# Kernel tuning notes

Hardware: AMD Instinct MI355X
Metric: run time of the kernel (lower is better)

## Reference

```python
import jax, jax.numpy as jnp
import numpy as np

K = 3          # kernel size
SH, SW = 2, 1  # stride
PH, PW = 1, 1  # padding


def conv2d(x, w, b, stride, pad):
    y = jax.lax.conv_general_dilated(
        x, w, window_strides=stride,
        padding=[(pad[0], pad[0]), (pad[1], pad[1])],
        dimension_numbers=('NCHW', 'OIHW', 'NCHW'))
    return y + b[None, :, None, None]


def setup_inputs() -> dict:
    key = jax.random.key(0)
    ks = jax.random.split(key, 4)
    x = jax.random.normal(ks[0], (8, 64, 128, 128), jnp.float32)
    # scale offset weights small so sampled offsets are O(1) pixels (exercises
    # the bilinear path without sampling far out of bounds)
    w_offset = jax.random.normal(ks[1], (18, 64, 3, 3), jnp.float32) * 0.02
    b_offset = jnp.zeros((18,), jnp.float32)
    w_mask = jax.random.normal(ks[2], (9, 64, 3, 3), jnp.float32) * 0.05
    b_mask = jnp.zeros((9,), jnp.float32)
    w_conv = jax.random.normal(ks[3], (64, 64, 3, 3), jnp.float32) * (1.0 / 24.0)
    return dict(x=x, w_offset=w_offset, b_offset=b_offset,
                w_mask=w_mask, b_mask=b_mask, w_conv=w_conv)


def _bilinear_gather(x, py, px):
    # x: [B,C,H,W]; py, px: [B,K2,Ho,Wo] float sampling coordinates.
    # Zero-padding outside the image (torchvision deform_conv2d semantics).
    B, C, H, W = x.shape
    y0f = jnp.floor(py)
    x0f = jnp.floor(px)
    dy = py - y0f
    dx = px - x0f
    y0 = y0f.astype(jnp.int32)
    x0 = x0f.astype(jnp.int32)

    def corner(yi, xi, wgt):
        valid = (yi >= 0) & (yi < H) & (xi >= 0) & (xi < W)
        yc = jnp.clip(yi, 0, H - 1)
        xc = jnp.clip(xi, 0, W - 1)
        # per-batch fancy gather -> [B, C, K2, Ho, Wo]
        g = jax.vmap(lambda xb, yb, xbi: xb[:, yb, xbi])(x, yc, xc)
        return g * (wgt * valid)[:, None]

    return (corner(y0,     x0,     (1 - dy) * (1 - dx))
            + corner(y0,     x0 + 1, (1 - dy) * dx)
            + corner(y0 + 1, x0,     dy * (1 - dx))
            + corner(y0 + 1, x0 + 1, dy * dx))


def reference(x, w_offset, b_offset, w_mask, b_mask, w_conv):
    B, C, H, W = x.shape
    offset = conv2d(x, w_offset, b_offset, (SH, SW), (PH, PW))   # [B, 2*K2, Ho, Wo]
    mask = jax.nn.sigmoid(conv2d(x, w_mask, b_mask, (SH, SW), (PH, PW)))  # [B, K2, Ho, Wo]
    Ho, Wo = offset.shape[2], offset.shape[3]
    K2 = K * K
    off = offset.reshape(B, K2, 2, Ho, Wo)
    off_y = off[:, :, 0]   # [B,K2,Ho,Wo]
    off_x = off[:, :, 1]
    ky = (jnp.arange(K2) // K).astype(jnp.float32)
    kx = (jnp.arange(K2) % K).astype(jnp.float32)
    hs = (jnp.arange(Ho) * SH - PH).astype(jnp.float32)
    ws = (jnp.arange(Wo) * SW - PW).astype(jnp.float32)
    py = off_y + ky[None, :, None, None] + hs[None, None, :, None]
    px = off_x + kx[None, :, None, None] + ws[None, None, None, :]
    sampled = _bilinear_gather(x, py, px) * mask[:, None]  # [B,C,K2,Ho,Wo]
    # weighted accumulate over in-channels and kernel taps
    out = jnp.einsum('ock,bckhw->bohw', w_conv.reshape(-1, C, K2), sampled)
    return out
```

## Files before the change

### kernel.cpp

```cpp
#include <hip/hip_runtime.h>
#include <hip/hip_fp16.h>
#include <math.h>

#define BB 8
#define CC 64
#define HH 128
#define WW 128
#define HO 64
#define WO 128
#define OC 64
#define HW (HH * WW)

typedef __attribute__((ext_vector_type(4))) float floatx4;
typedef __attribute__((ext_vector_type(8))) _Float16 half8;

__device__ __forceinline__ unsigned short f2h(float f) {
    __half h = __float2half(f);
    return __builtin_bit_cast(unsigned short, h);
}
__device__ __forceinline__ unsigned int packpair(float a, float b) {
    __half2 h = __floats2half2_rn(a, b);
    return __builtin_bit_cast(unsigned int, h);
}
__device__ __forceinline__ void lgkm_barrier() {
    asm volatile("s_waitcnt lgkmcnt(0)" ::: "memory");
    __builtin_amdgcn_s_barrier();
}

__global__ __launch_bounds__(256) void prep(
    const float* __restrict__ x,
    const float* __restrict__ w_off, const float* __restrict__ w_msk,
    const float* __restrict__ w_conv,
    unsigned int* __restrict__ xP,
    unsigned short* __restrict__ Wom, unsigned short* __restrict__ W2)
{
    __shared__ float T[64][77];
    int tid = threadIdx.x, bx = blockIdx.x;
    if (bx < 2048) {
        int wh = bx & 1, b = (bx >> 1) & 7, y = bx >> 4;
        int w0 = wh << 6;
        const float* xb = x + (((size_t)b * CC) * HH + y) * WW + w0;
#pragma unroll
        for (int i = 0; i < 4; ++i) {
            int idx = i * 256 + tid;
            int cch = idx >> 4, f4 = (idx & 15) << 2;
            floatx4 v = *(const floatx4*)(xb + (size_t)cch * HW + f4);
            T[cch][f4 + 0] = v.x;
            T[cch][f4 + 1] = v.y;
            T[cch][f4 + 2] = v.z;
            T[cch][f4 + 3] = v.w;
        }
        if (tid < 64) {
            float e = 0.0f;
            if (w0 + 64 < WW) e = xb[(size_t)tid * HW + 64];
            T[tid][64] = e;
        }
        __syncthreads();
        int ch = tid & 63;
        int wb = (tid >> 6) << 4;
        size_t base = ((((size_t)b * HH + y) * WW) + w0 + wb) * 64 + ch;
#pragma unroll
        for (int j = 0; j < 4; ++j) {
            int wl = wb + 4 * j;
            float a0 = T[ch][wl + 0];
            float a1 = T[ch][wl + 1];
            float a2 = T[ch][wl + 2];
            float a3 = T[ch][wl + 3];
            float a4 = T[ch][wl + 4];
            xP[base + (size_t)(4 * j + 0) * 64] = packpair(a0, a1);
            xP[base + (size_t)(4 * j + 1) * 64] = packpair(a1, a2);
            xP[base + (size_t)(4 * j + 2) * 64] = packpair(a2, a3);
            xP[base + (size_t)(4 * j + 3) * 64] = packpair(a3, a4);
        }
    } else if (bx < 2120) {
        int i = (bx - 2048) * 256 + tid;
        int chn = i / 576, kk = i % 576;
        int xs = kk >> 6, cc = kk & 63;
        float v = 0.0f;
        if (chn < 18)      v = w_off[(chn * CC + cc) * 9 + xs];
        else if (chn < 27) v = w_msk[((chn - 18) * CC + cc) * 9 + xs];
        Wom[i] = f2h(v);
    } else {
        int i = (bx - 2120) * 256 + tid;
        int k = i % 9, cc = (i / 9) % CC, o = i / (CC * 9);
        W2[((size_t)k * OC + o) * CC + cc] = f2h(w_conv[i]);
    }
}

__global__ __launch_bounds__(256, 4) void fused(
    const unsigned int* __restrict__ xP,
    const unsigned short* __restrict__ Wom, const unsigned short* __restrict__ W2,
    const float* __restrict__ b_off, const float* __restrict__ b_msk,
    float* __restrict__ out)
{
    __shared__ __align__(16) char lds[18304];
    typedef _Float16 XsRow[34][72];
    XsRow* Xs = (XsRow*)lds;
    unsigned short (*S)[32][64] = (unsigned short(*)[32][64])lds;
    uint2* metaC = (uint2*)(lds + 8192);
    uint2* metaR = (uint2*)(lds + 10496);
    float (*omr)[33] = (float(*)[33])(lds + 14720);

    int tid = threadIdx.x;
    int lane = tid & 63;
    int wv = __builtin_amdgcn_readfirstlane(tid >> 6);
    int bx = blockIdx.x;
    int b = bx & 7;
    int rest = bx >> 3;
    int h = rest >> 2;
    int w0 = (rest & 3) * 32;
    int h2 = 2 * h - 1;
    int m16 = lane & 15, q = lane >> 4;

    const unsigned int* xPb_u = xP + (size_t)b * HW * 64;

    for (int u = tid; u < 1632; u += 256) {
        int ky = u / 544;
        int rem = u - ky * 544;
        int col = rem >> 4, c4 = rem & 15;
        int hy = h2 + ky, wc = w0 - 1 + col;
        unsigned int lo0 = 0u, lo1 = 0u;
        if ((unsigned)hy < (unsigned)HH && (unsigned)wc < (unsigned)WW) {
            const uint4 g = *(const uint4*)(xPb_u + ((size_t)hy * WW + wc) * 64 + c4 * 4);
            lo0 = (g.x & 0xffffu) | (g.y << 16);
            lo1 = (g.z & 0xffffu) | (g.w << 16);
        }
        uint2* dst = (uint2*)((unsigned short*)lds + ((ky * 34 + col) * 72 + c4 * 4));
        *dst = make_uint2(lo0, lo1);
    }
    lgkm_barrier();

    {
        int mt = wv & 1, nt = wv >> 1;
        floatx4 a = (floatx4){0.f, 0.f, 0.f, 0.f};
        const _Float16* wa = (const _Float16*)Wom + (mt * 16 + m16) * 576 + q * 8;
#pragma unroll
        for (int t = 0; t < 18; ++t) {
            int xs = t >> 1, ky = xs / 3, kx = xs % 3;
            half8 af = *(const half8*)(wa + t * 32);
            half8 bf = *(const half8*)&Xs[ky][nt * 16 + m16 + kx][(t & 1) * 32 + q * 8];
            a = __builtin_amdgcn_mfma_f32_16x16x32_f16(af, bf, a, 0, 0, 0);
        }
#pragma unroll
        for (int r = 0; r < 4; ++r) {
            int chn = mt * 16 + q * 4 + r;
            if (chn < 27) omr[chn][nt * 16 + m16] = a[r];
        }
    }
    lgkm_barrier();

    for (int u = tid; u < 288; u += 256) {
        int kk = u >> 5, pos = u & 31;
        float offy = omr[2 * kk][pos] + b_off[2 * kk];
        float offx = omr[2 * kk + 1][pos] + b_off[2 * kk + 1];
        float mk = 1.0f / (1.0f + __expf(-(omr[18 + kk][pos] + b_msk[kk])));
        float py = offy + (float)(kk / 3) + (float)h2;
        float px = offx + (float)(kk % 3) + (float)(w0 + pos - 1);

        float y0f = floorf(py), x0f = floorf(px);
        float dy = py - y0f, dx = px - x0f;
        int y0 = (int)y0f, x0 = (int)x0f;
        int y1 = y0 + 1, x1 = x0 + 1;
        bool vy0 = (unsigned)y0 < (unsigned)HH;
        bool vy1 = (unsigned)y1 < (unsigned)HH;
        bool vx0 = (unsigned)x0 < (unsigned)WW;
        bool vx1 = (unsigned)x1 < (unsigned)WW;
        float w00 = (1.0f - dy) * (1.0f - dx) * ((vy0 && vx0) ? mk : 0.0f);
        float w01 = (1.0f - dy) * dx          * ((vy0 && vx1) ? mk : 0.0f);
        float w10 = dy * (1.0f - dx)          * ((vy1 && vx0) ? mk : 0.0f);
        float w11 = dy * dx                   * ((vy1 && vx1) ? mk : 0.0f);
        int xbase = min(max(x0, 0), WW - 2);
        bool s0 = x0 > xbase;
        bool s1 = x1 > xbase;
        float cxA = (s0 ? 0.f : w00) + (s1 ? 0.f : w01);
        float cyA = (s0 ? w00 : 0.f) + (s1 ? w01 : 0.f);
        float cxB = (s0 ? 0.f : w10) + (s1 ? 0.f : w11);
        float cyB = (s0 ? w10 : 0.f) + (s1 ? w11 : 0.f);
        int yc0 = min(max(y0, 0), HH - 1);
        int yc1 = min(max(y1, 0), HH - 1);

        __half2 hA = __floats2half2_rn(cxA, cyA);
        __half2 hB = __floats2half2_rn(cxB, cyB);
        metaC[u] = make_uint2(__builtin_bit_cast(unsigned int, hA),
                              __builtin_bit_cast(unsigned int, hB));
        metaR[u] = make_uint2((unsigned)(yc0 * WW + xbase) * 256u,
                              (unsigned)(yc1 * WW + xbase) * 256u);
    }
    lgkm_barrier();

    int p0 = wv * 8;
    const char* xPb = (const char*)xPb_u;
    unsigned int voff = 4u * (unsigned)lane;
    floatx4 acc0 = (floatx4){0.f, 0.f, 0.f, 0.f};
    floatx4 acc1 = (floatx4){0.f, 0.f, 0.f, 0.f};

    unsigned int Ga0[8], Ga1[8], Gb0[8], Gb1[8];

    auto issue = [&](int k, unsigned int (&A0)[8], unsigned int (&A1)[8]) {
#pragma unroll
        for (int i = 0; i < 8; ++i) {
            uint2 zw = metaR[k * 32 + p0 + i];
            const char* r0 = xPb + (unsigned)__builtin_amdgcn_readfirstlane((int)zw.x);
            const char* r1 = xPb + (unsigned)__builtin_amdgcn_readfirstlane((int)zw.y);
            A0[i] = *(const unsigned int*)(r0 + voff);
            A1[i] = *(const unsigned int*)(r1 + voff);
        }
    };
    auto dostore = [&](int k, int buf, unsigned int (&A0)[8], unsigned int (&A1)[8]) {
#pragma unroll
        for (int i = 0; i < 8; ++i) {
            uint2 cf = metaC[k * 32 + p0 + i];
            __half2 hA = __builtin_bit_cast(__half2, cf.x);
            __half2 hB = __builtin_bit_cast(__half2, cf.y);
            __half2 g0 = __builtin_bit_cast(__half2, A0[i]);
            __half2 g1 = __builtin_bit_cast(__half2, A1[i]);
            __half2 p = __hfma2(hA, g0, __hmul2(hB, g1));
            __half sv = __hadd(__low2half(p), __high2half(p));
            int pos = p0 + i;
            S[buf][pos][((lane >> 3) ^ (pos & 7)) * 8 + (lane & 7)] =
                __builtin_bit_cast(unsigned short, sv);
        }
    };
    auto mfma_step = [&](int k, int buf) {
        const _Float16* wk = (const _Float16*)W2
            + ((size_t)(k * OC) + wv * 16 + m16) * CC + q * 8;
#pragma unroll
        for (int s = 0; s < 2; ++s) {
            half8 af = *(const half8*)(wk + s * 32);
            int cb = ((q + 4 * s) ^ (m16 & 7)) * 8;
            half8 bf0 = *(const half8*)&S[buf][m16][cb];
            half8 bf1 = *(const half8*)&S[buf][16 + m16][cb];
            acc0 = __builtin_amdgcn_mfma_f32_16x16x32_f16(af, bf0, acc0, 0, 0, 0);
            acc1 = __builtin_amdgcn_mfma_f32_16x16x32_f16(af, bf1, acc1, 0, 0, 0);
        }
    };

    issue(0, Ga0, Ga1);
    dostore(0, 0, Ga0, Ga1);
    issue(1, Gb0, Gb1);
#pragma unroll
    for (int k = 0; k < 9; ++k) {
        lgkm_barrier();
        mfma_step(k, k & 1);
        if ((k & 1) == 0) {
            if (k < 7) issue(k + 2, Ga0, Ga1);
            if (k < 8) dostore(k + 1, (k + 1) & 1, Gb0, Gb1);
        } else {
            if (k < 7) issue(k + 2, Gb0, Gb1);
            if (k < 8) dostore(k + 1, (k + 1) & 1, Ga0, Ga1);
        }
    }

#pragma unroll
    for (int nt = 0; nt < 2; ++nt) {
        floatx4 av = nt ? acc1 : acc0;
#pragma unroll
        for (int r = 0; r < 4; ++r) {
            int o = wv * 16 + q * 4 + r;
            out[(((size_t)b * OC + o) * HO + h) * WO + w0 + nt * 16 + m16] = av[r];
        }
    }
}

extern "C" void kernel_launch(void* const* d_in, const int* in_sizes, int n_in,
                              void* d_out, int out_size, void* d_ws, size_t ws_size,
                              hipStream_t stream)
{
    const float* x      = (const float*)d_in[0];
    const float* w_off  = (const float*)d_in[1];
    const float* b_off  = (const float*)d_in[2];
    const float* w_msk  = (const float*)d_in[3];
    const float* b_msk  = (const float*)d_in[4];
    const float* w_conv = (const float*)d_in[5];
    float* out = (float*)d_out;

    unsigned int* xP = (unsigned int*)d_ws;
    unsigned short* Wom = (unsigned short*)(xP + (size_t)BB * HW * 64);
    unsigned short* W2 = Wom + 32 * 576;

    prep<<<dim3(2264), dim3(256), 0, stream>>>(x, w_off, w_msk, w_conv,
                                               xP, Wom, W2);
    fused<<<dim3(2048), dim3(256), 0, stream>>>(xP, Wom, W2,
                                                b_off, b_msk, out);
}
```

Before: 145.6 us.

## Widen fused tile to 64 pixels with per-wave private sample staging

```diff
diff --git a/kernel.cpp b/kernel.cpp
--- a/kernel.cpp
+++ b/kernel.cpp
@@ -93,13 +93,11 @@
     const float* __restrict__ b_off, const float* __restrict__ b_msk,
     float* __restrict__ out)
 {
-    __shared__ __align__(16) char lds[18304];
-    typedef _Float16 XsRow[34][72];
-    XsRow* Xs = (XsRow*)lds;
-    unsigned short (*S)[32][64] = (unsigned short(*)[32][64])lds;
-    uint2* metaC = (uint2*)(lds + 8192);
-    uint2* metaR = (uint2*)(lds + 10496);
-    float (*omr)[33] = (float(*)[33])(lds + 14720);
+    __shared__ __align__(16) char lds[35968];
+    _Float16* XsH = (_Float16*)lds;
+    float* omr = (float*)(lds + 28544);
+    uint2* metaR = (uint2*)lds;
+    uint2* metaC = (uint2*)(lds + 4608);
 
     int tid = threadIdx.x;
     int lane = tid & 63;
@@ -107,16 +105,16 @@
     int bx = blockIdx.x;
     int b = bx & 7;
     int rest = bx >> 3;
-    int h = rest >> 2;
-    int w0 = (rest & 3) * 32;
+    int h = rest >> 1;
+    int w0 = (rest & 1) << 6;
     int h2 = 2 * h - 1;
     int m16 = lane & 15, q = lane >> 4;
 
     const unsigned int* xPb_u = xP + (size_t)b * HW * 64;
 
-    for (int u = tid; u < 1632; u += 256) {
-        int ky = u / 544;
-        int rem = u - ky * 544;
+    for (int u = tid; u < 3168; u += 256) {
+        int ky = u / 1056;
+        int rem = u - ky * 1056;
         int col = rem >> 4, c4 = rem & 15;
         int hy = h2 + ky, wc = w0 - 1 + col;
         unsigned int lo0 = 0u, lo1 = 0u;
@@ -125,35 +123,40 @@
             lo0 = (g.x & 0xffffu) | (g.y << 16);
             lo1 = (g.z & 0xffffu) | (g.w << 16);
         }
-        uint2* dst = (uint2*)((unsigned short*)lds + ((ky * 34 + col) * 72 + c4 * 4));
-        *dst = make_uint2(lo0, lo1);
+        *(uint2*)(XsH + (ky * 66 + col) * 72 + c4 * 4) = make_uint2(lo0, lo1);
     }
     lgkm_barrier();
 
     {
-        int mt = wv & 1, nt = wv >> 1;
-        floatx4 a = (floatx4){0.f, 0.f, 0.f, 0.f};
-        const _Float16* wa = (const _Float16*)Wom + (mt * 16 + m16) * 576 + q * 8;
+        int nt = wv;
+        floatx4 a0 = (floatx4){0.f, 0.f, 0.f, 0.f};
+        floatx4 a1 = (floatx4){0.f, 0.f, 0.f, 0.f};
+        const _Float16* wa0 = (const _Float16*)Wom + m16 * 576 + q * 8;
+        const _Float16* wa1 = wa0 + 16 * 576;
 #pragma unroll
         for (int t = 0; t < 18; ++t) {
             int xs = t >> 1, ky = xs / 3, kx = xs % 3;
-            half8 af = *(const half8*)(wa + t * 32);
-            half8 bf = *(const half8*)&Xs[ky][nt * 16 + m16 + kx][(t & 1) * 32 + q * 8];
-            a = __builtin_amdgcn_mfma_f32_16x16x32_f16(af, bf, a, 0, 0, 0);
+            half8 bf = *(const half8*)(XsH + (ky * 66 + nt * 16 + m16 + kx) * 72
+                                       + (t & 1) * 32 + q * 8);
+            half8 af0 = *(const half8*)(wa0 + t * 32);
+            half8 af1 = *(const half8*)(wa1 + t * 32);
+            a0 = __builtin_amdgcn_mfma_f32_16x16x32_f16(af0, bf, a0, 0, 0, 0);
+            a1 = __builtin_amdgcn_mfma_f32_16x16x32_f16(af1, bf, a1, 0, 0, 0);
         }
 #pragma unroll
         for (int r = 0; r < 4; ++r) {
-            int chn = mt * 16 + q * 4 + r;
-            if (chn < 27) omr[chn][nt * 16 + m16] = a[r];
+            int c0 = q * 4 + r;
+            omr[c0 * 68 + nt * 16 + m16] = a0[r];
+            if (c0 + 16 < 27) omr[(c0 + 16) * 68 + nt * 16 + m16] = a1[r];
         }
     }
     lgkm_barrier();
 
-    for (int u = tid; u < 288; u += 256) {
-        int kk = u >> 5, pos = u & 31;
-        float offy = omr[2 * kk][pos] + b_off[2 * kk];
-        float offx = omr[2 * kk + 1][pos] + b_off[2 * kk + 1];
-        float mk = 1.0f / (1.0f + __expf(-(omr[18 + kk][pos] + b_msk[kk])));
+    for (int u = tid; u < 576; u += 256) {
+        int kk = u >> 6, pos = u & 63;
+        float offy = omr[(2 * kk) * 68 + pos] + b_off[2 * kk];
+        float offx = omr[(2 * kk + 1) * 68 + pos] + b_off[2 * kk + 1];
+        float mk = 1.0f / (1.0f + __expf(-(omr[(18 + kk) * 68 + pos] + b_msk[kk])));
         float py = offy + (float)(kk / 3) + (float)h2;
         float px = offx + (float)(kk % 3) + (float)(w0 + pos - 1);
 
@@ -188,78 +191,87 @@
     }
     lgkm_barrier();
 
-    int p0 = wv * 8;
+    int pw0 = wv * 16;
+    int p = lane & 31;
+    int ph = lane >> 5;
+    unsigned int voffC = 8u * (unsigned)p;
     const char* xPb = (const char*)xPb_u;
-    unsigned int voff = 4u * (unsigned)lane;
-    floatx4 acc0 = (floatx4){0.f, 0.f, 0.f, 0.f};
-    floatx4 acc1 = (floatx4){0.f, 0.f, 0.f, 0.f};
-
-    unsigned int Ga0[8], Ga1[8], Gb0[8], Gb1[8];
-
-    auto issue = [&](int k, unsigned int (&A0)[8], unsigned int (&A1)[8]) {
+    char* Sw = lds + 9216 + wv * 2048;
+
+    floatx4 acc[4];
+#pragma unroll
+    for (int m = 0; m < 4; ++m) acc[m] = (floatx4){0.f, 0.f, 0.f, 0.f};
+
+    half8 A[8];
+    uint2 G0[8], G1[8];
+
+    auto loadA = [&](int k) {
+#pragma unroll
+        for (int m = 0; m < 4; ++m)
+#pragma unroll
+            for (int ks = 0; ks < 2; ++ks)
+                A[m * 2 + ks] = *(const half8*)((const _Float16*)W2
+                    + ((size_t)(k * OC + m * 16 + m16)) * CC + ks * 32 + q * 8);
+    };
+    auto issueG = [&](int k) {
 #pragma unroll
         for (int i = 0; i < 8; ++i) {
-            uint2 zw = metaR[k * 32 + p0 + i];
-            const char* r0 = xPb + (unsigned)__builtin_amdgcn_readfirstlane((int)zw.x);
-            const char* r1 = xPb + (unsigned)__builtin_amdgcn_readfirstlane((int)zw.y);
-            A0[i] = *(const unsigned int*)(r0 + voff);
-            A1[i] = *(const unsigned int*)(r1 + voff);
-        }
-    };
-    auto dostore = [&](int k, int buf, unsigned int (&A0)[8], unsigned int (&A1)[8]) {
+            uint2 zw = metaR[k * 64 + pw0 + ph * 8 + i];
+            G0[i] = *(const uint2*)(xPb + (zw.x + voffC));
+            G1[i] = *(const uint2*)(xPb + (zw.y + voffC));
+        }
+    };
+    auto blend = [&](int k) {
 #pragma unroll
         for (int i = 0; i < 8; ++i) {
-            uint2 cf = metaC[k * 32 + p0 + i];
+            int rw = ph * 8 + i;
+            uint2 cf = metaC[k * 64 + pw0 + rw];
             __half2 hA = __builtin_bit_cast(__half2, cf.x);
             __half2 hB = __builtin_bit_cast(__half2, cf.y);
-            __half2 g0 = __builtin_bit_cast(__half2, A0[i]);
-            __half2 g1 = __builtin_bit_cast(__half2, A1[i]);
-            __half2 p = __hfma2(hA, g0, __hmul2(hB, g1));
-            __half sv = __hadd(__low2half(p), __high2half(p));
-            int pos = p0 + i;
-            S[buf][pos][((lane >> 3) ^ (pos & 7)) * 8 + (lane & 7)] =
-                __builtin_bit_cast(unsigned short, sv);
-        }
-    };
-    auto mfma_step = [&](int k, int buf) {
-        const _Float16* wk = (const _Float16*)W2
-            + ((size_t)(k * OC) + wv * 16 + m16) * CC + q * 8;
-#pragma unroll
-        for (int s = 0; s < 2; ++s) {
-            half8 af = *(const half8*)(wk + s * 32);
-            int cb = ((q + 4 * s) ^ (m16 & 7)) * 8;
-            half8 bf0 = *(const half8*)&S[buf][m16][cb];
-            half8 bf1 = *(const half8*)&S[buf][16 + m16][cb];
-            acc0 = __builtin_amdgcn_mfma_f32_16x16x32_f16(af, bf0, acc0, 0, 0, 0);
-            acc1 = __builtin_amdgcn_mfma_f32_16x16x32_f16(af, bf1, acc1, 0, 0, 0);
-        }
-    };
-
-    issue(0, Ga0, Ga1);
-    dostore(0, 0, Ga0, Ga1);
-    issue(1, Gb0, Gb1);
+            __half2 t0 = __hfma2(hA, __builtin_bit_cast(__half2, G0[i].x),
+                                 __hmul2(hB, __builtin_bit_cast(__half2, G1[i].x)));
+            __half2 t1 = __hfma2(hA, __builtin_bit_cast(__half2, G0[i].y),
+                                 __hmul2(hB, __builtin_bit_cast(__half2, G1[i].y)));
+            __half v0 = __hadd(__low2half(t0), __high2half(t0));
+            __half v1 = __hadd(__low2half(t1), __high2half(t1));
+            unsigned int d = (unsigned int)__builtin_bit_cast(unsigned short, v0)
+                           | ((unsigned int)__builtin_bit_cast(unsigned short, v1) << 16);
+            int cbi = p >> 2;
+            *(unsigned int*)(Sw + rw * 128 + ((cbi ^ (rw & 7)) * 16 + (p & 3) * 4)) = d;
+        }
+    };
+    auto mfma_tap = [&]() {
+        half8 Bf[2];
+#pragma unroll
+        for (int ks = 0; ks < 2; ++ks) {
+            int cbi = ks * 4 + q;
+            Bf[ks] = *(const half8*)(Sw + m16 * 128 + ((cbi ^ (m16 & 7)) * 16));
+        }
+#pragma unroll
+        for (int m = 0; m < 4; ++m)
+#pragma unroll
+            for (int ks = 0; ks < 2; ++ks)
+                acc[m] = __builtin_amdgcn_mfma_f32_16x16x32_f16(A[m * 2 + ks], Bf[ks],
+                                                                acc[m], 0, 0, 0);
+    };
+
+    loadA(0);
+    issueG(0);
 #pragma unroll
     for (int k = 0; k < 9; ++k) {
-        lgkm_barrier();
-        mfma_step(k, k & 1);
-        if ((k & 1) == 0) {
-            if (k < 7) issue(k + 2, Ga0, Ga1);
-            if (k < 8) dostore(k + 1, (k + 1) & 1, Gb0, Gb1);
-        } else {
-            if (k < 7) issue(k + 2, Gb0, Gb1);
-            if (k < 8) dostore(k + 1, (k + 1) & 1, Ga0, Ga1);
-        }
-    }
-
-#pragma unroll
-    for (int nt = 0; nt < 2; ++nt) {
-        floatx4 av = nt ? acc1 : acc0;
+        blend(k);
+        if (k < 8) issueG(k + 1);
+        mfma_tap();
+        if (k < 8) loadA(k + 1);
+    }
+
+#pragma unroll
+    for (int m = 0; m < 4; ++m)
 #pragma unroll
         for (int r = 0; r < 4; ++r) {
-            int o = wv * 16 + q * 4 + r;
-            out[(((size_t)b * OC + o) * HO + h) * WO + w0 + nt * 16 + m16] = av[r];
-        }
-    }
+            int o = m * 16 + q * 4 + r;
+            out[(((size_t)b * OC + o) * HO + h) * WO + w0 + pw0 + m16] = acc[m][r];
+        }
 }
 
 extern "C" void kernel_launch(void* const* d_in, const int* in_sizes, int n_in,
@@ -280,6 +292,6 @@
 
     prep<<<dim3(2264), dim3(256), 0, stream>>>(x, w_off, w_msk, w_conv,
                                                xP, Wom, W2);
-    fused<<<dim3(2048), dim3(256), 0, stream>>>(xP, Wom, W2,
+    fused<<<dim3(1024), dim3(256), 0, stream>>>(xP, Wom, W2,
                                                 b_off, b_msk, out);
 }
```

Result: slower. 173.4 us (+19.1%).
